# Kernel optimization log

Measured on AMD Instinct MI355X. Metric: run time of the kernel, lower is better.

The kernel has to match this reference:

```python
import jax, jax.numpy as jnp
import numpy as np

N_SRC = 100000
N_DST = 100000
E = 1250000
IN_SRC = 64
IN_DST = 64
OUT = 64


def setup_inputs() -> dict:
    key = jax.random.key(0)
    k = jax.random.split(key, 7)
    x_src = jax.random.normal(k[0], (N_SRC, IN_SRC), dtype=jnp.float32)
    x_dst = jax.random.normal(k[1], (N_DST, IN_DST), dtype=jnp.float32)
    edge_index_sd = jax.random.randint(k[2], (2, E), 0, N_SRC, dtype=jnp.int64)
    edge_weight = jax.random.uniform(k[3], (E,), dtype=jnp.float32)
    # Linear params (torch: y = x @ W.T + b), kaiming-ish scale
    W_nei = jax.random.normal(k[4], (OUT, IN_SRC), dtype=jnp.float32) / np.sqrt(IN_SRC)
    W_self = jax.random.normal(k[5], (OUT, IN_DST), dtype=jnp.float32) / np.sqrt(IN_DST)
    b_self = jax.random.normal(k[6], (OUT,), dtype=jnp.float32) / np.sqrt(IN_DST)
    return {"x_src": x_src, "x_dst": x_dst, "edge_index_sd": edge_index_sd,
            "edge_weight": edge_weight, "W_nei": W_nei, "W_self": W_self,
            "b_self": b_self}


def reference(x_src, x_dst, edge_index_sd, edge_weight, W_nei, W_self, b_self):
    src_idx = edge_index_sd[0]
    dst_idx = edge_index_sd[1]
    # self term: [N_dst, out]
    out = x_dst @ W_self.T + b_self
    # neighbor transform then gather per edge: [E, out]
    h_src = x_src @ W_nei.T
    msg = h_src[src_idx] * edge_weight[:, None]
    # scatter-add into dst rows
    out = out.at[dst_idx].add(msg)
    return out
```

## Files before the change

kernel.cpp:

```cpp
#include <hip/hip_runtime.h>

#define NN 100000
#define FD 64
#define NE 1250000

#define RPB 128
#define NBK ((NN + RPB - 1) / RPB)
#define NBP 1024
#define CAP 2048
#define CH  8192
#define NCH ((NE + CH - 1) / CH)
#define NTILE (NN / 16)

#define TPW 2
#define NWM (NTILE / TPW)
#define LIN_GRID ((2 * NWM + 3) / 4)

typedef __attribute__((ext_vector_type(8))) short bf16x8;
typedef __attribute__((ext_vector_type(4))) float f32x4;

__device__ __forceinline__ short cvt_bf16(float f) {
    unsigned u = __float_as_uint(f);
    return (short)((u + 0x7FFFu + ((u >> 16) & 1u)) >> 16);
}
__device__ __forceinline__ float bf2f(unsigned short u) {
    return __uint_as_float(((unsigned)u) << 16);
}

__global__ __launch_bounds__(256) void lin_both(
    const float* __restrict__ x_src, const float* __restrict__ x_dst,
    const float* __restrict__ W_nei, const float* __restrict__ W_self,
    const float* __restrict__ b_self, unsigned short* __restrict__ hbuf,
    float* __restrict__ out, int* __restrict__ gcur)
{
    if (gcur && blockIdx.x == 0) {
        #pragma unroll
        for (int i = 0; i < NBP / 256; i++) gcur[threadIdx.x + i * 256] = 0;
    }
    const int lane = threadIdx.x & 63;
    const int m    = lane & 15;
    const int quad = lane >> 4;
    const int gw   = blockIdx.x * 4 + (threadIdx.x >> 6);
    if (gw >= 2 * NWM) return;
    const bool self = gw >= NWM;
    const int  wm   = self ? gw - NWM : gw;
    const float* __restrict__ x = self ? x_dst : x_src;
    const float* __restrict__ W = self ? W_self : W_nei;

    const float* xb = x + (size_t)(wm * (TPW * 16) + m) * FD;
    float4 xv[TPW][4];
    #pragma unroll
    for (int t = 0; t < TPW; t++) {
        const float* xr = xb + (size_t)t * 16 * FD;
        xv[t][0] = *(const float4*)(xr + quad * 8);
        xv[t][1] = *(const float4*)(xr + quad * 8 + 4);
        xv[t][2] = *(const float4*)(xr + 32 + quad * 8);
        xv[t][3] = *(const float4*)(xr + 32 + quad * 8 + 4);
    }

    bf16x8 wf[2][4];
    #pragma unroll
    for (int kc = 0; kc < 2; kc++) {
        #pragma unroll
        for (int ct = 0; ct < 4; ct++) {
            const float4 w0 = *(const float4*)(W + (ct * 16 + m) * FD + kc * 32 + quad * 8);
            const float4 w1 = *(const float4*)(W + (ct * 16 + m) * FD + kc * 32 + quad * 8 + 4);
            bf16x8 f;
            f[0]=cvt_bf16(w0.x); f[1]=cvt_bf16(w0.y); f[2]=cvt_bf16(w0.z); f[3]=cvt_bf16(w0.w);
            f[4]=cvt_bf16(w1.x); f[5]=cvt_bf16(w1.y); f[6]=cvt_bf16(w1.z); f[7]=cvt_bf16(w1.w);
            wf[kc][ct] = f;
        }
    }

    float4 bv[4];
    if (self) {
        #pragma unroll
        for (int ct = 0; ct < 4; ct++)
            bv[ct] = *(const float4*)(b_self + ct * 16 + quad * 4);
    }

    #pragma unroll
    for (int t = 0; t < TPW; t++) {
        bf16x8 a0, a1;
        a0[0]=cvt_bf16(xv[t][0].x); a0[1]=cvt_bf16(xv[t][0].y);
        a0[2]=cvt_bf16(xv[t][0].z); a0[3]=cvt_bf16(xv[t][0].w);
        a0[4]=cvt_bf16(xv[t][1].x); a0[5]=cvt_bf16(xv[t][1].y);
        a0[6]=cvt_bf16(xv[t][1].z); a0[7]=cvt_bf16(xv[t][1].w);
        a1[0]=cvt_bf16(xv[t][2].x); a1[1]=cvt_bf16(xv[t][2].y);
        a1[2]=cvt_bf16(xv[t][2].z); a1[3]=cvt_bf16(xv[t][2].w);
        a1[4]=cvt_bf16(xv[t][3].x); a1[5]=cvt_bf16(xv[t][3].y);
        a1[6]=cvt_bf16(xv[t][3].z); a1[7]=cvt_bf16(xv[t][3].w);

        f32x4 acc[4];
        #pragma unroll
        for (int ct = 0; ct < 4; ct++) {
            f32x4 z = (f32x4){0.f, 0.f, 0.f, 0.f};
            z = __builtin_amdgcn_mfma_f32_16x16x32_bf16(wf[0][ct], a0, z, 0, 0, 0);
            z = __builtin_amdgcn_mfma_f32_16x16x32_bf16(wf[1][ct], a1, z, 0, 0, 0);
            acc[ct] = z;
        }

        const size_t rowbase = (size_t)(wm * (TPW * 16) + t * 16 + m) * FD;
        if (!self) {
            #pragma unroll
            for (int ct = 0; ct < 4; ct++) {
                ushort4 sv;
                sv.x = (unsigned short)cvt_bf16(acc[ct][0]);
                sv.y = (unsigned short)cvt_bf16(acc[ct][1]);
                sv.z = (unsigned short)cvt_bf16(acc[ct][2]);
                sv.w = (unsigned short)cvt_bf16(acc[ct][3]);
                *(ushort4*)(hbuf + rowbase + ct * 16 + quad * 4) = sv;
            }
        } else {
            #pragma unroll
            for (int ct = 0; ct < 4; ct++) {
                float4 v;
                v.x = acc[ct][0] + bv[ct].x;
                v.y = acc[ct][1] + bv[ct].y;
                v.z = acc[ct][2] + bv[ct].z;
                v.w = acc[ct][3] + bv[ct].w;
                *(float4*)(out + rowbase + ct * 16 + quad * 4) = v;
            }
        }
    }
}

__global__ __launch_bounds__(1024) void kplace(
    const int* __restrict__ src, const int* __restrict__ dst,
    const float* __restrict__ ew, int* __restrict__ gcursor,
    int2* __restrict__ sp)
{
    __shared__ int cnt[NBP];
    const int t = threadIdx.x;
    if (t < NBP) cnt[t] = 0;
    __syncthreads();
    const int e0 = blockIdx.x * CH;

    int d[8];
    #pragma unroll
    for (int k = 0; k < 8; k++) {
        const int e = e0 + t + k * 1024;
        d[k] = (e < NE) ? dst[e] : -1;
    }
    #pragma unroll
    for (int k = 0; k < 8; k++)
        if (d[k] >= 0) atomicAdd(&cnt[d[k] >> 7], 1);
    __syncthreads();

    if (t < NBP) {
        const int c = cnt[t];
        cnt[t] = c ? (t * CAP + atomicAdd(&gcursor[t], c)) : 0;
    }
    __syncthreads();

    int s[8]; float w[8];
    #pragma unroll
    for (int k = 0; k < 8; k++) {
        const int e = e0 + t + k * 1024;
        if (e < NE) { s[k] = src[e]; w[k] = ew[e]; }
    }
    #pragma unroll
    for (int k = 0; k < 8; k++) {
        if (d[k] >= 0) {
            const int p = atomicAdd(&cnt[d[k] >> 7], 1);
            sp[p] = make_int2(s[k] | ((d[k] & (RPB - 1)) << 17),
                              __float_as_int(w[k]));
        }
    }
}

__global__ __launch_bounds__(512) void sort_gather(
    const int2* __restrict__ sp, const int* __restrict__ gcursor,
    const unsigned short* __restrict__ h, float* __restrict__ out)
{
    __shared__ int2 ebuf[CAP + 16];
    __shared__ int hist[RPB];
    __shared__ int rs[RPB];
    __shared__ int cur[RPB];
    const int t = threadIdx.x;
    const int b = blockIdx.x;
    const int cnt = gcursor[b];
    const int s0 = b * CAP;

    if (t < RPB) hist[t] = 0;

    int2 ev[4]; int er[4];
    #pragma unroll
    for (int k = 0; k < 4; k++) {
        const int j = t + k * 512;
        if (j < cnt) { ev[k] = sp[s0 + j]; er[k] = ev[k].x >> 17; }
        else er[k] = -1;
    }
    __syncthreads();
    #pragma unroll
    for (int k = 0; k < 4; k++)
        if (er[k] >= 0) atomicAdd(&hist[er[k]], 1);
    __syncthreads();
    if (t < 64) {
        const int v0 = hist[2*t], v1 = hist[2*t + 1];
        const int s = v0 + v1;
        int inc = s;
        #pragma unroll
        for (int off = 1; off < 64; off <<= 1) {
            int u = __shfl_up(inc, off, 64);
            if (t >= off) inc += u;
        }
        const int ex = inc - s;
        rs[2*t]      = ex;       cur[2*t]     = ex;
        rs[2*t + 1]  = ex + v0;  cur[2*t + 1] = ex + v0;
    }
    __syncthreads();
    #pragma unroll
    for (int k = 0; k < 4; k++) {
        if (er[k] >= 0) {
            const int p = atomicAdd(&cur[er[k]], 1);
            ebuf[p] = ev[k];
        }
    }
    if (t < 16) ebuf[cnt + t] = make_int2(0, 0);
    __syncthreads();

    const int wv   = t >> 6;
    const int lane = t & 63;
    const int q    = lane >> 4;
    const int tc   = lane & 15;
    const unsigned tb = (unsigned)tc << 3;
    const int row0 = b * RPB;

    for (int i = 0; i < 16; i++) {
        const int r   = wv + i * 8;
        const int row = row0 + r;
        if (row >= NN) break;
        const int rsr = rs[r];
        const int n   = hist[r];
        float a0 = 0.f, a1 = 0.f, a2 = 0.f, a3 = 0.f;
        for (int k = 0; k < n; k += 16) {
            int2 ed[4];
            #pragma unroll
            for (int j = 0; j < 4; j++)
                ed[j] = ebuf[rsr + k + j * 4 + q];
            uint2 dv[4]; float wv4[4];
            #pragma unroll
            for (int j = 0; j < 4; j++) {
                const unsigned off = (((unsigned)(ed[j].x & 0x1FFFF)) << 7) | tb;
                dv[j] = *(const uint2*)((const char*)h + off);
                wv4[j] = (k + j * 4 + q < n) ? __int_as_float(ed[j].y) : 0.f;
            }
            #pragma unroll
            for (int j = 0; j < 4; j++) {
                const float w = wv4[j];
                a0 = fmaf(__uint_as_float(dv[j].x << 16),         w, a0);
                a1 = fmaf(__uint_as_float(dv[j].x & 0xFFFF0000u), w, a1);
                a2 = fmaf(__uint_as_float(dv[j].y << 16),         w, a2);
                a3 = fmaf(__uint_as_float(dv[j].y & 0xFFFF0000u), w, a3);
            }
        }
        a0 += __shfl_xor(a0, 16, 64); a1 += __shfl_xor(a1, 16, 64);
        a2 += __shfl_xor(a2, 16, 64); a3 += __shfl_xor(a3, 16, 64);
        a0 += __shfl_xor(a0, 32, 64); a1 += __shfl_xor(a1, 32, 64);
        a2 += __shfl_xor(a2, 32, 64); a3 += __shfl_xor(a3, 32, 64);
        if (q == 0) {
            float4* p = (float4*)(out + (size_t)row * FD + (tc << 2));
            float4 v = *p;
            v.x += a0; v.y += a1; v.z += a2; v.w += a3;
            *p = v;
        }
    }
}

__global__ __launch_bounds__(256) void scatter_edges(
    const unsigned short* __restrict__ h, const int* __restrict__ eidx,
    const float* __restrict__ ew, float* __restrict__ out)
{
    const int lane  = threadIdx.x & 63;
    const int gwave = (int)((blockIdx.x * blockDim.x + threadIdx.x) >> 6);
    const int nwave = (int)((gridDim.x * blockDim.x) >> 6);
    const int* __restrict__ src = eidx;
    const int* __restrict__ dst = eidx + NE;
    for (int e = gwave; e < NE; e += nwave) {
        const float v = bf2f(h[(size_t)src[e] * FD + lane]) * ew[e];
        atomicAdd(out + (size_t)dst[e] * FD + lane, v);
    }
}

extern "C" void kernel_launch(void* const* d_in, const int* in_sizes, int n_in,
                              void* d_out, int out_size, void* d_ws, size_t ws_size,
                              hipStream_t stream)
{
    const float* x_src  = (const float*)d_in[0];
    const float* x_dst  = (const float*)d_in[1];
    const int*   eidx   = (const int*)  d_in[2];
    const float* ew     = (const float*)d_in[3];
    const float* W_nei  = (const float*)d_in[4];
    const float* W_self = (const float*)d_in[5];
    const float* b_self = (const float*)d_in[6];
    float* out = (float*)d_out;

    const int* src = eidx;
    const int* dst = eidx + NE;

    char* ws = (char*)d_ws;
    size_t off = 0;
    auto alloc = [&](size_t bytes) { char* p = ws + off; off += (bytes + 15) & ~(size_t)15; return p; };
    unsigned short* h = (unsigned short*)alloc((size_t)NN * FD * sizeof(unsigned short));
    int*  gcursor  = (int*) alloc((size_t)NBP * sizeof(int));
    int2* sp       = (int2*)alloc((size_t)NBP * CAP * sizeof(int2));
    const size_t need_main = off;
    const size_t need_h    = (size_t)NN * FD * sizeof(unsigned short);

    if (ws_size >= need_main) {
        lin_both<<<LIN_GRID, 256, 0, stream>>>(x_src, x_dst, W_nei, W_self,
                                               b_self, h, out, gcursor);
        kplace<<<NCH, 1024, 0, stream>>>(src, dst, ew, gcursor, sp);
        sort_gather<<<NBK, 512, 0, stream>>>(sp, gcursor, h, out);
    } else if (ws_size >= need_h) {
        lin_both<<<LIN_GRID, 256, 0, stream>>>(x_src, x_dst, W_nei, W_self,
                                               b_self, h, out, nullptr);
        scatter_edges<<<2048, 256, 0, stream>>>(h, eidx, ew, out);
    }
}
```

Before: 172.1 us.

## Fuse linear transform and edge bucketing into one heterogeneous kernel launch

Merges the dense linear kernel and the edge placement (bucket by destination) kernel into a single launch. The first blocks do edge placement with 256 threads and 16 edges per thread, and the remaining blocks do the MFMA linear transform. The cursor zeroing moves to a hipMemsetAsync. This removes a kernel boundary and lets the memory-bound bucketing overlap with the linear compute. The cost is an extra memset launch, and the cursor atomics now come from more, smaller blocks.

```diff
diff --git a/kernel.cpp b/kernel.cpp
--- a/kernel.cpp
+++ b/kernel.cpp
@@ -8,14 +8,17 @@
 #define NBK ((NN + RPB - 1) / RPB)
 #define NBP 1024
 #define CAP 2048
-#define CH  8192
-#define NCH ((NE + CH - 1) / CH)
 #define NTILE (NN / 16)
 
 #define TPW 2
 #define NWM (NTILE / TPW)
 #define LIN_GRID ((2 * NWM + 3) / 4)
 
+#define EPT 16
+#define CH2 (256 * EPT)
+#define NCH2 ((NE + CH2 - 1) / CH2)
+#define FUSE_GRID (NCH2 + LIN_GRID)
+
 typedef __attribute__((ext_vector_type(8))) short bf16x8;
 typedef __attribute__((ext_vector_type(4))) float f32x4;
 
@@ -27,21 +30,14 @@
     return __uint_as_float(((unsigned)u) << 16);
 }
 
-__global__ __launch_bounds__(256) void lin_both(
+__device__ __forceinline__ void lin_wave(
     const float* __restrict__ x_src, const float* __restrict__ x_dst,
     const float* __restrict__ W_nei, const float* __restrict__ W_self,
     const float* __restrict__ b_self, unsigned short* __restrict__ hbuf,
-    float* __restrict__ out, int* __restrict__ gcur)
-{
-    if (gcur && blockIdx.x == 0) {
-        #pragma unroll
-        for (int i = 0; i < NBP / 256; i++) gcur[threadIdx.x + i * 256] = 0;
-    }
-    const int lane = threadIdx.x & 63;
+    float* __restrict__ out, int gw, int lane)
+{
     const int m    = lane & 15;
     const int quad = lane >> 4;
-    const int gw   = blockIdx.x * 4 + (threadIdx.x >> 6);
-    if (gw >= 2 * NWM) return;
     const bool self = gw >= NWM;
     const int  wm   = self ? gw - NWM : gw;
     const float* __restrict__ x = self ? x_dst : x_src;
@@ -125,48 +121,74 @@
     }
 }
 
-__global__ __launch_bounds__(1024) void kplace(
+__global__ __launch_bounds__(256) void lin_place(
+    const float* __restrict__ x_src, const float* __restrict__ x_dst,
+    const float* __restrict__ W_nei, const float* __restrict__ W_self,
+    const float* __restrict__ b_self, unsigned short* __restrict__ hbuf,
+    float* __restrict__ out,
     const int* __restrict__ src, const int* __restrict__ dst,
     const float* __restrict__ ew, int* __restrict__ gcursor,
     int2* __restrict__ sp)
 {
     __shared__ int cnt[NBP];
-    const int t = threadIdx.x;
-    if (t < NBP) cnt[t] = 0;
-    __syncthreads();
-    const int e0 = blockIdx.x * CH;
-
-    int d[8];
-    #pragma unroll
-    for (int k = 0; k < 8; k++) {
-        const int e = e0 + t + k * 1024;
-        d[k] = (e < NE) ? dst[e] : -1;
-    }
-    #pragma unroll
-    for (int k = 0; k < 8; k++)
-        if (d[k] >= 0) atomicAdd(&cnt[d[k] >> 7], 1);
-    __syncthreads();
-
-    if (t < NBP) {
-        const int c = cnt[t];
-        cnt[t] = c ? (t * CAP + atomicAdd(&gcursor[t], c)) : 0;
-    }
-    __syncthreads();
-
-    int s[8]; float w[8];
-    #pragma unroll
-    for (int k = 0; k < 8; k++) {
-        const int e = e0 + t + k * 1024;
-        if (e < NE) { s[k] = src[e]; w[k] = ew[e]; }
-    }
-    #pragma unroll
-    for (int k = 0; k < 8; k++) {
-        if (d[k] >= 0) {
-            const int p = atomicAdd(&cnt[d[k] >> 7], 1);
-            sp[p] = make_int2(s[k] | ((d[k] & (RPB - 1)) << 17),
-                              __float_as_int(w[k]));
-        }
-    }
+    if (blockIdx.x < NCH2) {
+        const int t = threadIdx.x;
+        #pragma unroll
+        for (int i = 0; i < NBP / 256; i++) cnt[t + i * 256] = 0;
+        __syncthreads();
+        const int e0 = blockIdx.x * CH2;
+
+        int d[EPT];
+        #pragma unroll
+        for (int k = 0; k < EPT; k++) {
+            const int e = e0 + t + k * 256;
+            d[k] = (e < NE) ? dst[e] : -1;
+        }
+        #pragma unroll
+        for (int k = 0; k < EPT; k++)
+            if (d[k] >= 0) atomicAdd(&cnt[d[k] >> 7], 1);
+        __syncthreads();
+
+        #pragma unroll
+        for (int i = 0; i < NBP / 256; i++) {
+            const int bb = t + i * 256;
+            const int c = cnt[bb];
+            cnt[bb] = c ? (bb * CAP + atomicAdd(&gcursor[bb], c)) : 0;
+        }
+        __syncthreads();
+
+        int s[EPT]; float w[EPT];
+        #pragma unroll
+        for (int k = 0; k < EPT; k++) {
+            const int e = e0 + t + k * 256;
+            if (e < NE) { s[k] = src[e]; w[k] = ew[e]; }
+        }
+        #pragma unroll
+        for (int k = 0; k < EPT; k++) {
+            if (d[k] >= 0) {
+                const int p = atomicAdd(&cnt[d[k] >> 7], 1);
+                sp[p] = make_int2(s[k] | ((d[k] & (RPB - 1)) << 17),
+                                  __float_as_int(w[k]));
+            }
+        }
+        return;
+    }
+    const int gw = (blockIdx.x - NCH2) * 4 + (threadIdx.x >> 6);
+    if (gw >= 2 * NWM) return;
+    lin_wave(x_src, x_dst, W_nei, W_self, b_self, hbuf, out,
+             gw, threadIdx.x & 63);
+}
+
+__global__ __launch_bounds__(256) void lin_both(
+    const float* __restrict__ x_src, const float* __restrict__ x_dst,
+    const float* __restrict__ W_nei, const float* __restrict__ W_self,
+    const float* __restrict__ b_self, unsigned short* __restrict__ hbuf,
+    float* __restrict__ out)
+{
+    const int gw = blockIdx.x * 4 + (threadIdx.x >> 6);
+    if (gw >= 2 * NWM) return;
+    lin_wave(x_src, x_dst, W_nei, W_self, b_self, hbuf, out,
+             gw, threadIdx.x & 63);
 }
 
 __global__ __launch_bounds__(512) void sort_gather(
@@ -309,13 +331,14 @@
     const size_t need_h    = (size_t)NN * FD * sizeof(unsigned short);
 
     if (ws_size >= need_main) {
-        lin_both<<<LIN_GRID, 256, 0, stream>>>(x_src, x_dst, W_nei, W_self,
-                                               b_self, h, out, gcursor);
-        kplace<<<NCH, 1024, 0, stream>>>(src, dst, ew, gcursor, sp);
+        hipMemsetAsync(gcursor, 0, (size_t)NBP * sizeof(int), stream);
+        lin_place<<<FUSE_GRID, 256, 0, stream>>>(x_src, x_dst, W_nei, W_self,
+                                                 b_self, h, out, src, dst, ew,
+                                                 gcursor, sp);
         sort_gather<<<NBK, 512, 0, stream>>>(sp, gcursor, h, out);
     } else if (ws_size >= need_h) {
         lin_both<<<LIN_GRID, 256, 0, stream>>>(x_src, x_dst, W_nei, W_self,
-                                               b_self, h, out, nullptr);
+                                               b_self, h, out);
         scatter_edges<<<2048, 256, 0, stream>>>(h, eidx, ew, out);
     }
 }
```

New measurement: 174.5 us. No clear change (+1.4%).
